# Optimization experiments

Measured on AMD Instinct MI355X. Metric: run time of the kernel, lower is better.

## Reference

```python
import jax, jax.numpy as jnp
import numpy as np

LMAX = 6; MMAX = 2
C = 128          # num_channels
H = 8            # num_heads
ALPHA = 32       # attn_alpha_channels
VAL = 16         # attn_value_channels (H*VAL == C)
HID = 64         # attn_hidden_channels
FFN = 128        # ffn_hidden_channels
NL = 4           # num_layers
CUTOFF = 12.0; NRBF = 600
AVG_DEG = 23.395238876342773
AVG_NODES = 77.81317
EPS = 1e-16

def _maps():
    idx, ls = [], []
    for l in range(LMAX + 1):
        mm = min(l, MMAX)
        for m in range(-mm, mm + 1):
            idx.append(l * l + l + m); ls.append(l)
    return np.array(idx), np.array(ls)
_M2F_np, _LOF_np = _maps()
M2F = jnp.asarray(_M2F_np)   # [KM] full-coefficient index of each m-restricted coeff
LOF = jnp.asarray(_LOF_np)   # [KM] degree l of each m-restricted coeff
KM = int(_M2F_np.shape[0])   # 29 for lmax=6, mmax=2
KF = (LMAX + 1) ** 2         # 49

def _rbf(d):
    # GaussianSmearing(0, cutoff, NRBF, width_scalar=2.0)
    off = jnp.linspace(0.0, CUTOFF, NRBF)
    coeff = -0.5 / (2.0 * (off[1] - off[0])) ** 2
    return jnp.exp(coeff * (d[:, None] - off) ** 2)

def _envelope(d):
    # PolynomialEnvelope, exponent p=5
    x = d / CUTOFF
    env = 1.0 - 21.0 * x ** 5 + 35.0 * x ** 6 - 15.0 * x ** 7
    return jnp.where(x < 1.0, env, 0.0)

def _rms(x, g):
    # merge-norm over channel dim with learned per-channel scale
    return x * jax.lax.rsqrt(jnp.mean(x * x, axis=-1, keepdims=True) + 1e-6) * g

def _forward(atomic_numbers, edge_index, edge_distance, emb,
             We0, be0, We1, be1, Weproj, gamma1, gamma2,
             Wr0, Wr1, Wrl, Wmsg, Wap, wa, Wg, Wv, Wo,
             Wf1, Wfg, Wf2, Wh1, Wh2):
    N = atomic_numbers.shape[0]
    src, tgt = edge_index[0], edge_index[1]
    rbf = _rbf(edge_distance)            # [E, NRBF]
    env = _envelope(edge_distance)       # [E]
    # node init: atom embedding on the l=0 component
    x = jnp.zeros((N, KF, C), rbf.dtype).at[:, 0, :].set(emb[atomic_numbers])
    # edge-degree embedding: radial MLP -> per-edge coeffs -> scatter to targets
    h = jax.nn.silu(rbf @ We0 + be0)
    h = jax.nn.silu(h @ We1 + be1)
    deg = (h @ Weproj).reshape(-1, KM, C)              # [E, KM, C]
    x = x.at[tgt[:, None], M2F[None, :], :].add(deg / AVG_DEG)
    for i in range(NL):
        # ---- equivariant graph attention ----
        y = _rms(x, gamma1[i])
        ym = y[:, M2F, :]                               # [N, KM, C] m-restricted
        m = jnp.concatenate([ym[src], ym[tgt]], axis=-1)  # [E, KM, 2C]
        m = jnp.einsum('ekc,ch->ekh', m, Wmsg[i])       # [E, KM, HID]
        # radial function, shared across m within each l (use_rad_l_parametrization)
        rad = jax.nn.silu(jax.nn.silu(rbf @ Wr0[i]) @ Wr1[i])
        radl = rad @ Wrl[i]                             # [E, LMAX+1]
        m = m * radl[:, LOF][..., None]
        # attention logits from invariant (l=0) part
        a = jax.nn.silu(m[:, 0, :] @ Wap[i]).reshape(-1, H, ALPHA)
        logits = jnp.einsum('eha,ha->eh', a, wa[i])     # [E, H]
        segmax = jnp.full((N, H), -jnp.inf, logits.dtype).at[tgt].max(logits)
        ex = env[:, None] * jnp.exp(logits - segmax[tgt])  # envelope-masked softmax
        den = jax.ops.segment_sum(ex, tgt, num_segments=N)
        attn = ex / (den[tgt] + EPS)                    # [E, H]
        # SwiGLU-gated equivariant values
        g = jax.nn.silu(m[:, 0, :] @ Wg[i])             # [E, H*VAL]
        v = jnp.einsum('ekh,hv->ekv', m, Wv[i]) * g[:, None, :]
        v = v.reshape(-1, KM, H, VAL) * attn[:, None, :, None]
        agg = jax.ops.segment_sum(v.reshape(-1, KM, H * VAL), tgt, num_segments=N)
        out = jnp.einsum('nkv,vc->nkc', agg, Wo[i])     # [N, KM, C]
        x = x.at[:, M2F, :].add(out)
        # ---- feed-forward (grid-MLP style SwiGLU) ----
        y = _rms(x, gamma2[i])
        gf = jax.nn.silu(y[:, 0, :] @ Wfg[i])           # [N, FFN]
        hf = jnp.einsum('nkc,cf->nkf', y, Wf1[i]) * gf[:, None, :]
        x = x + jnp.einsum('nkf,fc->nkc', hf, Wf2[i])
    # energy head on invariant part, sum-aggregated over nodes
    s = jax.nn.silu(x[:, 0, :] @ Wh1) @ Wh2             # [N, 1]
    return (jnp.sum(s) / AVG_NODES).reshape(1)

def setup_inputs() -> dict:
    key = jax.random.key(0)
    ks = jax.random.split(key, 24)
    N, E = 6000, 120000
    def rn(k, shape, scale=0.05):
        return jax.random.normal(k, shape, dtype=jnp.float32) * scale
    inp = {}
    inp['atomic_numbers'] = jax.random.randint(ks[0], (N,), 0, 128)
    inp['edge_index'] = jax.random.randint(ks[1], (2, E), 0, N)
    inp['edge_distance'] = jax.random.uniform(ks[2], (E,), minval=0.5, maxval=CUTOFF, dtype=jnp.float32)
    inp['emb'] = rn(ks[3], (128, C), 1.0)
    inp['We0'] = rn(ks[4], (NRBF, 128)); inp['be0'] = jnp.zeros((128,), jnp.float32)
    inp['We1'] = rn(ks[5], (128, 128)); inp['be1'] = jnp.zeros((128,), jnp.float32)
    inp['Weproj'] = rn(ks[6], (128, KM * C))
    inp['gamma1'] = jnp.ones((NL, C), jnp.float32)
    inp['gamma2'] = jnp.ones((NL, C), jnp.float32)
    inp['Wr0'] = rn(ks[7], (NL, NRBF, 128))
    inp['Wr1'] = rn(ks[8], (NL, 128, 128))
    inp['Wrl'] = rn(ks[9], (NL, 128, LMAX + 1), 0.1)
    inp['Wmsg'] = rn(ks[10], (NL, 2 * C, HID))
    inp['Wap'] = rn(ks[11], (NL, HID, H * ALPHA))
    inp['wa'] = rn(ks[12], (NL, H, ALPHA))
    inp['Wg'] = rn(ks[13], (NL, HID, H * VAL))
    inp['Wv'] = rn(ks[14], (NL, HID, H * VAL))
    inp['Wo'] = rn(ks[15], (NL, H * VAL, C))
    inp['Wf1'] = rn(ks[16], (NL, C, FFN))
    inp['Wfg'] = rn(ks[17], (NL, C, FFN))
    inp['Wf2'] = rn(ks[18], (NL, FFN, C))
    inp['Wh1'] = rn(ks[19], (C, C))
    inp['Wh2'] = rn(ks[20], (C, 1))
    return inp

def reference(atomic_numbers, edge_index, edge_distance, emb,
              We0, be0, We1, be1, Weproj, gamma1, gamma2,
              Wr0, Wr1, Wrl, Wmsg, Wap, wa, Wg, Wv, Wo,
              Wf1, Wfg, Wf2, Wh1, Wh2):
    return _forward(atomic_numbers, edge_index, edge_distance, emb,
                    We0, be0, We1, be1, Weproj, gamma1, gamma2,
                    Wr0, Wr1, Wrl, Wmsg, Wap, wa, Wg, Wv, Wo,
                    Wf1, Wfg, Wf2, Wh1, Wh2)
```

## Files before the change

### kernel.cpp

```cpp
#include <hip/hip_runtime.h>

#define KM 29
#define GTAB 2048

typedef __bf16 bf16_t;
typedef __bf16 bf16x8 __attribute__((ext_vector_type(8)));
typedef __bf16 bf16x4 __attribute__((ext_vector_type(4)));
typedef __bf16 bf16x2 __attribute__((ext_vector_type(2)));
typedef float  f32x4  __attribute__((ext_vector_type(4)));
typedef float  f32x2  __attribute__((ext_vector_type(2)));

__device__ __forceinline__ float silu_f(float x){ return x / (1.0f + __expf(-x)); }

__device__ __forceinline__ float wave_reduce_sum(float v){
  #pragma unroll
  for (int s = 1; s < 64; s <<= 1) v += __shfl_xor(v, s);
  return v;
}

__device__ __forceinline__ constexpr int LOF2(int k){
  return (k<1)?0 : (k<4)?1 : (k<9)?2 : (k<14)?3 : (k<19)?4 : (k<24)?5 : 6;
}

__device__ __forceinline__ f32x4 mfma16(bf16x8 a, bf16x8 b, f32x4 c){
// ... 136 lines not shown
    for (int l = 0; l < 7; l++) pl[l] = wave_reduce_sum(pl[l]);
    if (lane == 0){
      #pragma unroll
      for (int l = 0; l < 7; l++) radtab[(size_t)e*28 + i*7 + l] = pl[l];
    }
  }
}

__global__ void k_h2e(const float* __restrict__ ed, const float* __restrict__ h2tab,
                      bf16_t* __restrict__ h2e, int E){
  int idx = blockIdx.x*256 + threadIdx.x;
  if (idx >= E*128) return;
  int e = idx >> 7, ch = idx & 127;
  float d = ed[e];
  float u = d * ((GTAB-1)/12.0f);
  int j = (int)u; if (j > GTAB-2) j = GTAB-2;
  float f = u - (float)j;
  float a = h2tab[(size_t)j*128 + ch], b = h2tab[(size_t)(j+1)*128 + ch];
  h2e[idx] = (bf16_t)(a + f*(b-a));
}

__global__ __launch_bounds__(256) void k_h2sum(
    const bf16_t* __restrict__ h2e, const int* __restrict__ rowptr, const int* __restrict__ order,
    bf16_t* __restrict__ h2sum, int N)
{
  int n = blockIdx.x*2 + (threadIdx.x >> 7);
  int ch = threadIdx.x & 127;
  if (n >= N) return;
  int rp = rowptr[n], deg = rowptr[n+1] - rp;
  float acc = 0.f;
  for (int idx = 0; idx < deg; idx++){
    int e = order[rp+idx];
    acc += (float)h2e[(size_t)e*128 + ch];
  }
  h2sum[(size_t)n*128 + ch] = (bf16_t)acc;
}

__global__ __launch_bounds__(256) void k_init_x(
    const int* __restrict__ Z, const float* __restrict__ emb,
    const bf16_t* __restrict__ WeprojT, const bf16_t* __restrict__ h2sum,
    bf16_t* __restrict__ Xb, int N)
{
  __shared__ bf16_t h2s[32*136];
  __shared__ int Zs[32];
  int n0 = blockIdx.x*32, t = threadIdx.x;
  for (int idx = t; idx < 32*128; idx += 256){
    int nn = idx >> 7, ch = idx & 127;
    int n = n0 + nn;
    h2s[nn*136 + ch] = (n < N) ? h2sum[(size_t)n*128 + ch] : (bf16_t)0.f;
  }
  if (t < 32) Zs[t] = (n0 + t < N) ? Z[n0+t] : 0;
  __syncthreads();
  int wid = t >> 6, lane = t & 63;
  int mtile = wid & 1;
  int row = mtile*16 + (lane & 15);
  int koff = (lane >> 4)*8;
  bf16x8 afr[4];
  #pragma unroll
  for (int kk = 0; kk < 4; kk++) afr[kk] = *(const bf16x8*)(h2s + row*136 + kk*32 + koff);
  for (int nt = (wid>>1); nt < 232; nt += 2){
    f32x4 acc = {0.f,0.f,0.f,0.f};
    int col = nt*16 + (lane & 15);
    #pragma unroll
    for (int kk = 0; kk < 4; kk++){
      bf16x8 b = *(const bf16x8*)(WeprojT + (size_t)col*128 + kk*32 + koff);
      acc = mfma16(afr[kk], b, acc);
    }
    #pragma unroll
    for (int r = 0; r < 4; r++){
      int r32 = mtile*16 + (lane>>4)*4 + r;
      int n = n0 + r32;
      if (n < N){
        float v = acc[r] * (1.0f/23.395238876342773f);
        if (col < 128) v += emb[(size_t)Zs[r32]*128 + col];
        Xb[(size_t)n*3712 + col] = (bf16_t)v;
      }
    }
  }
}

__global__ __launch_bounds__(512) void k_pqv(
    const bf16_t* __restrict__ Xb, const float* __restrict__ gamma1,
    const bf16_t* __restrict__ WmsgCT, const bf16_t* __restrict__ WvT,
    unsigned char* __restrict__ PV8,
    float* __restrict__ P0, float* __restrict__ Q0, int layer)
{
  __shared__ bf16_t ys16[32*136];
  __shared__ bf16_t pq16[32*136];
  int n = blockIdx.x, t = threadIdx.x;
  int wid = t >> 6, lane = t & 63;
  const float* g1 = gamma1 + layer*128;
  const bf16_t* xp = Xb + (size_t)n*3712;
  for (int k = wid; k < KM; k += 8){
    float x0 = (float)xp[k*128 + lane], x1 = (float)xp[k*128 + 64 + lane];
    float ss = wave_reduce_sum(x0*x0 + x1*x1);
    float sc = rsqrtf(ss*(1.0f/128.0f) + 1e-6f);
    ys16[k*136 + lane]      = (bf16_t)(x0*sc*g1[lane]);
    ys16[k*136 + 64 + lane] = (bf16_t)(x1*sc*g1[64+lane]);
  }
  for (int idx = t; idx < 3*136; idx += 512) ys16[29*136 + idx] = (bf16_t)0.f;
  __syncthreads();
  int mtile = wid >> 2;
  int row = mtile*16 + (lane & 15);
  int koff = (lane >> 4)*8;
  {
    const bf16_t* Bc = WmsgCT + (size_t)layer*16384;
    f32x4 acc[2] = {{0,0,0,0},{0,0,0,0}};
    #pragma unroll
    for (int kk = 0; kk < 128; kk += 32){
      bf16x8 a = *(const bf16x8*)(ys16 + row*136 + kk + koff);
      #pragma unroll
      for (int u = 0; u < 2; u++){
        int col = ((wid&3)*2+u)*16 + (lane & 15);
        bf16x8 b = *(const bf16x8*)(Bc + (size_t)col*128 + kk + koff);
        acc[u] = mfma16(a, b, acc[u]);
      }
    }
    #pragma unroll
    for (int u = 0; u < 2; u++){
      int col = ((wid&3)*2+u)*16 + (lane & 15);
      #pragma unroll
      for (int r = 0; r < 4; r++){
        int r32 = mtile*16 + (lane>>4)*4 + r;
        pq16[r32*136 + col] = (bf16_t)acc[u][r];
      }
      if (mtile == 0 && (lane>>4) == 0){
        float v = acc[u][0];
        if (col < 64) P0[(size_t)n*64 + col] = v;
        else          Q0[(size_t)n*64 + col - 64] = v;
      }
    }
  }
  __syncthreads();
  {
    const bf16_t* Bt = WvT + (size_t)layer*8192;
    f32x4 acc[2] = {{0,0,0,0},{0,0,0,0}};
    #pragma unroll
    for (int kk = 0; kk < 64; kk += 32){
      bf16x8 a = *(const bf16x8*)(pq16 + row*136 + kk + koff);
      #pragma unroll
      for (int u = 0; u < 2; u++){
        int col = ((wid&3)*2+u)*16 + (lane & 15);
        bf16x8 b = *(const bf16x8*)(Bt + (size_t)col*64 + kk + koff);
        acc[u] = mfma16(a, b, acc[u]);
      }
    }
    unsigned char* pvp = PV8 + (size_t)n*4096;
    int r0i = mtile*16 + (lane>>4)*4;
    #pragma unroll
    for (int u = 0; u < 2; u++){
      int col = ((wid&3)*2+u)*16 + (lane & 15);
      float pk[4];
      #pragma unroll
      for (int r = 0; r < 4; r++){
        int r32 = r0i + r;
        pk[r] = (r32 < KM) ? acc[u][r] : 0.f;
      }
      int dw = __builtin_amdgcn_cvt_pk_fp8_f32(pk[0], pk[1], 0, false);
      dw = __builtin_amdgcn_cvt_pk_fp8_f32(pk[2], pk[3], dw, true);
      *(unsigned int*)(pvp + col*32 + r0i) = (unsigned int)dw;
    }
  }
}

__global__ __launch_bounds__(256) void k_edge_logits(
    const int* __restrict__ EI, const float* __restrict__ ed,
    const float* __restrict__ P0, const float* __restrict__ Q0,
    const float* __restrict__ radtab, const bf16_t* __restrict__ WapT, const float* __restrict__ wa,
    const bf16_t* __restrict__ WgT, float* __restrict__ logi, bf16_t* __restrict__ gate16,
    int E, int layer)
{
  __shared__ bf16_t m0s[16*72];
  __shared__ int   srcs[16], tgts[16];
  __shared__ float r0s[16];
  int t = threadIdx.x;
  int eb = blockIdx.x*16;
  if (t < 16){
    int e = eb + t;
    if (e < E){
      srcs[t] = EI[e]; tgts[t] = EI[E+e];
      float d = ed[e];
      float u = d * ((GTAB-1)/12.0f);
      int j = (int)u; if (j > GTAB-2) j = GTAB-2;
      float f = u - (float)j;
      float a = radtab[(size_t)j*28 + layer*7], b = radtab[(size_t)(j+1)*28 + layer*7];
      r0s[t] = a + f*(b-a);
    } else { srcs[t] = 0; tgts[t] = 0; r0s[t] = 0.f; }
  }
  __syncthreads();
  #pragma unroll
  for (int u = 0; u < 4; u++){
    int idx = t + u*256;
    int i = idx >> 6, j = idx & 63;
    m0s[i*72 + j] = (bf16_t)((P0[(size_t)srcs[i]*64 + j] + Q0[(size_t)tgts[i]*64 + j]) * r0s[i]);
  }
  __syncthreads();
  int wid = t >> 6, lane = t & 63;
  int l15 = lane & 15, lg = lane >> 4;
  int koff = lg*8;
  bf16x8 a0 = *(const bf16x8*)(m0s + l15*72 + koff);
  bf16x8 a1 = *(const bf16x8*)(m0s + l15*72 + 32 + koff);
  const bf16_t* Ba = WapT + (size_t)layer*16384;
  const bf16_t* Bg = WgT  + (size_t)layer*8192;
  const float* wav = wa + layer*256;
  f32x4 accA[4], accG[2];
  #pragma unroll
  for (int u = 0; u < 4; u++){
    int col = 64*wid + u*16 + l15;
    f32x4 acc = {0,0,0,0};
    acc = mfma16(a0, *(const bf16x8*)(Ba + (size_t)col*64 + koff), acc);
    acc = mfma16(a1, *(const bf16x8*)(Ba + (size_t)col*64 + 32 + koff), acc);
    accA[u] = acc;
  }
  #pragma unroll
  for (int u = 0; u < 2; u++){
    int col = 32*wid + u*16 + l15;
    f32x4 acc = {0,0,0,0};
    acc = mfma16(a0, *(const bf16x8*)(Bg + (size_t)col*64 + koff), acc);
    acc = mfma16(a1, *(const bf16x8*)(Bg + (size_t)col*64 + 32 + koff), acc);
    accG[u] = acc;
  }
  #pragma unroll
  for (int u = 0; u < 2; u++){
    int col = 32*wid + u*16 + l15;
    #pragma unroll
    for (int r = 0; r < 4; r++){
      int e = eb + lg*4 + r;
      if (e < E) gate16[(size_t)e*128 + col] = (bf16_t)silu_f(accG[u][r]);
    }
  }
  #pragma unroll
  for (int hpair = 0; hpair < 2; hpair++){
    int c0 = 64*wid + hpair*32 + l15;
    float w0 = wav[c0], w1 = wav[c0+16];
    float s[4];
    #pragma unroll
    for (int r = 0; r < 4; r++)
      s[r] = silu_f(accA[2*hpair][r])*w0 + silu_f(accA[2*hpair+1][r])*w1;
    #pragma unroll
    for (int r = 0; r < 4; r++){
      s[r] += __shfl_xor(s[r], 1);
      s[r] += __shfl_xor(s[r], 2);
      s[r] += __shfl_xor(s[r], 4);
      s[r] += __shfl_xor(s[r], 8);
    }
    if (l15 == 0){
      #pragma unroll
      for (int r = 0; r < 4; r++){
        int e = eb + lg*4 + r;
        if (e < E) logi[(size_t)e*8 + 2*wid + hpair] = s[r];
      }
    }
  }
}

#define FMA_DW(dw, kb) { \
  f32x2 lo_ = __builtin_amdgcn_cvt_pk_f32_fp8((dw), false); \
  f32x2 hi_ = __builtin_amdgcn_cvt_pk_f32_fp8((dw), true); \
  acc[(kb)]   += lo_.x * rw[LOF2((kb))]; \
  acc[(kb)+1] += lo_.y * rw[LOF2((kb)+1)]; \
  acc[(kb)+2] += hi_.x * rw[LOF2((kb)+2)]; \
  acc[(kb)+3] += hi_.y * rw[LOF2((kb)+3)]; }

__global__ __launch_bounds__(512, 4) void k_attn_ffn(
    const int* __restrict__ EI, const int* __restrict__ rowptr, const int* __restrict__ order,
    const float* __restrict__ ed,
    const bf16_t* __restrict__ WvT, const bf16_t* __restrict__ WoT,
    const unsigned char* __restrict__ PV8, const bf16_t* __restrict__ gate16,
    const float* __restrict__ logi, const float* __restrict__ radtab,
    const float* __restrict__ gamma1, const float* __restrict__ gamma2,
    const float* __restrict__ Wfg,
    const bf16_t* __restrict__ Wf1T, const bf16_t* __restrict__ Wf2T,
    const bf16_t* __restrict__ WmsgCT,
    bf16_t* __restrict__ Xb, int layer,
    unsigned char* __restrict__ PV8o, float* __restrict__ P0o, float* __restrict__ Q0o,
    int do_tail)
{
  __shared__ float  xs[3712];
  __shared__ bf16_t ysag[32*136];
  __shared__ bf16_t hsqv[32*136];
  __shared__ char   uA[4608];
  __shared__ int    esb[64], srcs[64];
  __shared__ float  denl[32];

  bf16_t* qm16 = (bf16_t*)uA;
  float*  at8  = (float*)uA;
  float*  rl7  = (float*)(uA + 2048);
  float*  pf   = (float*)uA;

  int n = blockIdx.x, t = threadIdx.x;
  int wid = t >> 6, lane = t & 63;
  int rp = rowptr[n], deg = rowptr[n+1] - rp;

  {
    const bf16x2* Xp2 = (const bf16x2*)(Xb + (size_t)n*3712);
    for (int p = t; p < 1856; p += 512){
      bf16x2 v = Xp2[p];
      xs[2*p]   = (float)v.x;
      xs[2*p+1] = (float)v.y;
    }
  }
  {
    int m0 = (deg < 64) ? deg : 64;
    if (t < m0){ int e = order[rp + t]; esb[t] = e; srcs[t] = EI[e]; }
  }
  __syncthreads();

  if (deg > 0){
    {
      const float* g1 = gamma1 + layer*128;
      for (int k = wid; k < KM; k += 8){
        float x0 = xs[k*128 + lane], x1 = xs[k*128 + 64 + lane];
        float ss = wave_reduce_sum(x0*x0 + x1*x1);
        float sc = rsqrtf(ss*(1.0f/128.0f) + 1e-6f);
        ysag[k*136 + lane]      = (bf16_t)(x0*sc*g1[lane]);
        ysag[k*136 + 64 + lane] = (bf16_t)(x1*sc*g1[64+lane]);
      }
      for (int idx = t; idx < 3*136; idx += 512) ysag[29*136 + idx] = (bf16_t)0.f;
    }
    __syncthreads();
    {
      const bf16_t* Bc = WmsgCT + (size_t)layer*16384 + (size_t)64*128;
      int mtile = wid >> 2;
      int col = (wid & 3)*16 + (lane & 15);
      int row = mtile*16 + (lane & 15);
      int koff = (lane >> 4)*8;
      f32x4 a2 = {0,0,0,0};
      #pragma unroll
      for (int kk = 0; kk < 128; kk += 32){
        bf16x8 a = *(const bf16x8*)(ysag + row*136 + kk + koff);
        bf16x8 b = *(const bf16x8*)(Bc + (size_t)col*128 + kk + koff);
        a2 = mfma16(a, b, a2);
      }
      #pragma unroll
      for (int r = 0; r < 4; r++){
        int r32 = mtile*16 + (lane>>4)*4 + r;
        qm16[r32*72 + col] = (bf16_t)a2[r];
      }
    }
    __syncthreads();
    {
      const bf16_t* Bt = WvT + (size_t)layer*8192;
      int mtile = wid >> 2, colt = (wid & 3)*2;
      int row = mtile*16 + (lane & 15);
      int koff = (lane >> 4)*8;
      f32x4 a2[2] = {{0,0,0,0},{0,0,0,0}};
      #pragma unroll
      for (int kk = 0; kk < 64; kk += 32){
        bf16x8 a = *(const bf16x8*)(qm16 + row*72 + kk + koff);
        #pragma unroll
        for (int u = 0; u < 2; u++){
          int col = (colt+u)*16 + (lane & 15);
          bf16x8 b = *(const bf16x8*)(Bt + (size_t)col*64 + kk + koff);
          a2[u] = mfma16(a, b, a2[u]);
        }
      }
      #pragma unroll
      for (int u = 0; u < 2; u++){
        int col = (colt+u)*16 + (lane & 15);
        #pragma unroll
        for (int r = 0; r < 4; r++){
          int r32 = mtile*16 + (lane>>4)*4 + r;
          hsqv[r32*136 + col] = (bf16_t)a2[u][r];
        }
      }
    }
    __syncthreads();
    int eg = t >> 7, hv = t & 127, h = hv >> 4;
    float acc[32];
    #pragma unroll
    for (int j = 0; j < 32; j++) acc[j] = 0.f;
    float S[7];
    #pragma unroll
    for (int l = 0; l < 7; l++) S[l] = 0.f;
    float dpart = 0.f;
    for (int base = 0; base < deg; base += 64){
      int ne = min(64, deg - base);
      if (base > 0){
        __syncthreads();
        if (t < ne){ int e = order[rp + base + t]; esb[t] = e; srcs[t] = EI[e]; }
        __syncthreads();
      }
      if (t < ne*8){
        int i = t >> 3, q = t & 7;
        int e = esb[i];
        float d = ed[e];
        at8[t] = env_f(d) * __expf(logi[(size_t)e*8 + q]);
        if (q < 7){
          float u = d * ((GTAB-1)/12.0f);
          int j = (int)u; if (j > GTAB-2) j = GTAB-2;
          float f = u - (float)j;
          float a = radtab[(size_t)j*28 + layer*7 + q], b = radtab[(size_t)(j+1)*28 + layer*7 + q];
          rl7[t] = a + f*(b-a);
        }
      }
      __syncthreads();
      uint4 A0 = {0,0,0,0}, A1 = {0,0,0,0}, B0 = {0,0,0,0}, B1 = {0,0,0,0};
      float gA = 0.f, gB = 0.f;
      int i = eg;
      if (i < ne){
        const uint4* p = (const uint4*)(PV8 + (size_t)srcs[i]*4096 + hv*32);
        A0 = p[0]; A1 = p[1];
        gA = (float)gate16[(size_t)esb[i]*128 + hv];
      }
      if (i + 4 < ne){
        const uint4* p = (const uint4*)(PV8 + (size_t)srcs[i+4]*4096 + hv*32);
        B0 = p[0]; B1 = p[1];
        gB = (float)gate16[(size_t)esb[i+4]*128 + hv];
      }
      while (i < ne){
        int i2 = i + 8;
        uint4 C0 = {0,0,0,0}, C1 = {0,0,0,0}; float gC = 0.f;
        if (i2 < ne){
          const uint4* p = (const uint4*)(PV8 + (size_t)srcs[i2]*4096 + hv*32);
          C0 = p[0]; C1 = p[1];
          gC = (float)gate16[(size_t)esb[i2]*128 + hv];
        }
        float ae = at8[i*8 + h];
        dpart += ae;
        float w = gA * ae;
        float rw[7];
        #pragma unroll
        for (int l = 0; l < 7; l++){ rw[l] = rl7[i*8 + l]*w; S[l] += rw[l]; }
        FMA_DW(A0.x, 0)  FMA_DW(A0.y, 4)  FMA_DW(A0.z, 8)  FMA_DW(A0.w, 12)
        FMA_DW(A1.x, 16) FMA_DW(A1.y, 20) FMA_DW(A1.z, 24) FMA_DW(A1.w, 28)
        A0 = B0; A1 = B1; gA = gB;
        B0 = C0; B1 = C1; gB = gC;
        i += 4;
      }
    }
    #pragma unroll
    for (int j = 0; j < 32; j++)
      acc[j] += (float)hsqv[j*136 + hv] * S[LOF2(j)];
    if ((hv & 15) == 0) denl[eg*8 + h] = dpart;
    __syncthreads();
    {
      float dsum = denl[h] + denl[8 + h] + denl[16 + h] + denl[24 + h];
      float inv = 1.0f/(dsum + 1e-30f);
      #pragma unroll
      for (int j = 0; j < 32; j++) acc[j] *= inv;
    }
    if (eg == 0){
      #pragma unroll
      for (int j = 0; j < 32; j++) ysag[j*136 + hv] = (bf16_t)acc[j];
    } else if (eg == 1){
      #pragma unroll
      for (int j = 0; j < 32; j++) hsqv[j*136 + hv] = (bf16_t)acc[j];
    }
    __syncthreads();
    if (eg == 2){
      #pragma unroll
      for (int j = 0; j < 32; j++) ysag[j*136 + hv] = (bf16_t)((float)ysag[j*136 + hv] + acc[j]);
    } else if (eg == 3){
      #pragma unroll
      for (int j = 0; j < 32; j++) hsqv[j*136 + hv] = (bf16_t)((float)hsqv[j*136 + hv] + acc[j]);
    }
    __syncthreads();
    for (int idx = t; idx < 32*128; idx += 512){
      int k = idx >> 7, c = idx & 127;
      ysag[k*136 + c] = (bf16_t)((float)ysag[k*136 + c] + (float)hsqv[k*136 + c]);
    }
    __syncthreads();
    {
      const bf16_t* Bt = WoT + (size_t)layer*16384;
      int mtile = wid >> 2, colt = (wid & 3)*2;
      int row = mtile*16 + (lane & 15);
      int koff = (lane >> 4)*8;
      f32x4 a2[2] = {{0,0,0,0},{0,0,0,0}};
      #pragma unroll
      for (int kk = 0; kk < 128; kk += 32){
        bf16x8 a = *(const bf16x8*)(ysag + row*136 + kk + koff);
        #pragma unroll
        for (int u = 0; u < 2; u++){
          int col = (colt+u)*16 + (lane & 15);
          bf16x8 b = *(const bf16x8*)(Bt + (size_t)col*128 + kk + koff);
          a2[u] = mfma16(a, b, a2[u]);
        }
      }
      #pragma unroll
      for (int u = 0; u < 2; u++){
        int col = (colt+u)*16 + (lane & 15);
        #pragma unroll
        for (int r = 0; r < 4; r++){
          int r32 = mtile*16 + (lane>>4)*4 + r;
          if (r32 < KM) xs[r32*128 + col] += a2[u][r];
        }
      }
    }
  }
  __syncthreads();
  const float* g2 = gamma2 + layer*128;
  for (int k = wid; k < KM; k += 8){
    float x0 = xs[k*128 + lane], x1 = xs[k*128 + 64 + lane];
    float ss = wave_reduce_sum(x0*x0 + x1*x1);
    float sc = rsqrtf(ss*(1.0f/128.0f) + 1e-6f);
    ysag[k*136 + lane]      = (bf16_t)(x0*sc*g2[lane]);
    ysag[k*136 + 64 + lane] = (bf16_t)(x1*sc*g2[64+lane]);
  }
  for (int idx = t; idx < 3*136; idx += 512) ysag[29*136 + idx] = (bf16_t)0.f;
  __syncthreads();
  {
    int part = t >> 7, f = t & 127;
    const float* Wfgp = Wfg + (size_t)layer*16384;
    float p = 0.f;
    for (int c = part*32; c < part*32 + 32; c++) p += (float)ysag[c] * Wfgp[c*128 + f];
    pf[part*128 + f] = p;
  }
  __syncthreads();
  if (t < 128) pf[512 + t] = silu_f(pf[t] + pf[128+t] + pf[256+t] + pf[384+t]);
  __syncthreads();
  {
    const bf16_t* Bt = Wf1T + (size_t)layer*16384;
    int mtile = wid >> 2, colt = (wid & 3)*2;
    int row = mtile*16 + (lane & 15);
    int koff = (lane >> 4)*8;
    f32x4 a2[2] = {{0,0,0,0},{0,0,0,0}};
    #pragma unroll
    for (int kk = 0; kk < 128; kk += 32){
      bf16x8 a = *(const bf16x8*)(ysag + row*136 + kk + koff);
      #pragma unroll
      for (int u = 0; u < 2; u++){
        int col = (colt+u)*16 + (lane & 15);
        bf16x8 b = *(const bf16x8*)(Bt + (size_t)col*128 + kk + koff);
        a2[u] = mfma16(a, b, a2[u]);
      }
    }
    #pragma unroll
    for (int u = 0; u < 2; u++){
      int col = (colt+u)*16 + (lane & 15);
      float gfc = pf[512 + col];
      #pragma unroll
      for (int r = 0; r < 4; r++){
        int r32 = mtile*16 + (lane>>4)*4 + r;
        hsqv[r32*136 + col] = (bf16_t)(a2[u][r]*gfc);
      }
    }
  }
  __syncthreads();
  {
    const bf16_t* Bt = Wf2T + (size_t)layer*16384;
    int mtile = wid >> 2, colt = (wid & 3)*2;
    int row = mtile*16 + (lane & 15);
    int koff = (lane >> 4)*8;
    f32x4 a2[2] = {{0,0,0,0},{0,0,0,0}};
    #pragma unroll
    for (int kk = 0; kk < 128; kk += 32){
      bf16x8 a = *(const bf16x8*)(hsqv + row*136 + kk + koff);
      #pragma unroll
      for (int u = 0; u < 2; u++){
        int col = (colt+u)*16 + (lane & 15);
        bf16x8 b = *(const bf16x8*)(Bt + (size_t)col*128 + kk + koff);
        a2[u] = mfma16(a, b, a2[u]);
      }
    }
    #pragma unroll
    for (int u = 0; u < 2; u++){
      int col = (colt+u)*16 + (lane & 15);
      #pragma unroll
      for (int r = 0; r < 4; r++){
        int r32 = mtile*16 + (lane>>4)*4 + r;
        if (r32 < KM) xs[r32*128 + col] += a2[u][r];
      }
    }
  }
  __syncthreads();
  {
    bf16x2* Xp2 = (bf16x2*)(Xb + (size_t)n*3712);
    for (int p = t; p < 1856; p += 512){
      bf16x2 v;
      v.x = (bf16_t)xs[2*p];
      v.y = (bf16_t)xs[2*p+1];
      Xp2[p] = v;
    }
  }
  if (do_tail){
    const float* g1n = gamma1 + (size_t)(layer+1)*128;
    for (int k = wid; k < KM; k += 8){
      float x0 = xs[k*128 + lane], x1 = xs[k*128 + 64 + lane];
      float ss = wave_reduce_sum(x0*x0 + x1*x1);
      float sc = rsqrtf(ss*(1.0f/128.0f) + 1e-6f);
      ysag[k*136 + lane]      = (bf16_t)(x0*sc*g1n[lane]);
      ysag[k*136 + 64 + lane] = (bf16_t)(x1*sc*g1n[64+lane]);
    }
    __syncthreads();
    int mtile = wid >> 2;
    int row = mtile*16 + (lane & 15);
    int koff = (lane >> 4)*8;
    {
      const bf16_t* Bc = WmsgCT + (size_t)(layer+1)*16384;
      f32x4 acc[2] = {{0,0,0,0},{0,0,0,0}};
      #pragma unroll
      for (int kk = 0; kk < 128; kk += 32){
        bf16x8 a = *(const bf16x8*)(ysag + row*136 + kk + koff);
        #pragma unroll
        for (int u = 0; u < 2; u++){
          int col = ((wid&3)*2+u)*16 + (lane & 15);
          bf16x8 b = *(const bf16x8*)(Bc + (size_t)col*128 + kk + koff);
          acc[u] = mfma16(a, b, acc[u]);
        }
      }
      #pragma unroll
      for (int u = 0; u < 2; u++){
        int col = ((wid&3)*2+u)*16 + (lane & 15);
        #pragma unroll
        for (int r = 0; r < 4; r++){
          int r32 = mtile*16 + (lane>>4)*4 + r;
          hsqv[r32*136 + col] = (bf16_t)acc[u][r];
        }
        if (mtile == 0 && (lane>>4) == 0){
          float v = acc[u][0];
          if (col < 64) P0o[(size_t)n*64 + col] = v;
          else          Q0o[(size_t)n*64 + col - 64] = v;
        }
      }
    }
    __syncthreads();
    {
      const bf16_t* Bt = WvT + (size_t)(layer+1)*8192;
      f32x4 acc[2] = {{0,0,0,0},{0,0,0,0}};
      #pragma unroll
      for (int kk = 0; kk < 64; kk += 32){
        bf16x8 a = *(const bf16x8*)(hsqv + row*136 + kk + koff);
        #pragma unroll
        for (int u = 0; u < 2; u++){
          int col = ((wid&3)*2+u)*16 + (lane & 15);
          bf16x8 b = *(const bf16x8*)(Bt + (size_t)col*64 + kk + koff);
          acc[u] = mfma16(a, b, acc[u]);
        }
      }
      unsigned char* pvp = PV8o + (size_t)n*4096;
      int r0i = mtile*16 + (lane>>4)*4;
      #pragma unroll
      for (int u = 0; u < 2; u++){
        int col = ((wid&3)*2+u)*16 + (lane & 15);
        float pk[4];
        #pragma unroll
        for (int r = 0; r < 4; r++){
          int r32 = r0i + r;
          pk[r] = (r32 < KM) ? acc[u][r] : 0.f;
        }
        int dw = __builtin_amdgcn_cvt_pk_fp8_f32(pk[0], pk[1], 0, false);
        dw = __builtin_amdgcn_cvt_pk_fp8_f32(pk[2], pk[3], dw, true);
        *(unsigned int*)(pvp + col*32 + r0i) = (unsigned int)dw;
      }
    }
  }
}

__global__ __launch_bounds__(256) void k_head(
    const bf16_t* __restrict__ Xb, const float* __restrict__ Wh1, const float* __restrict__ Wh2,
    float* __restrict__ partial, int N)
{
  __shared__ float wsum[4];
  int t = threadIdx.x;
  int half = t >> 7;
  int n = blockIdx.x*2 + half;
  int f = t & 127;
  float sv = 0.f;
  if (n < N){
    const bf16_t* xp = Xb + (size_t)n*3712;
    float acc = 0.f;
    for (int c = 0; c < 128; c++) acc += (float)xp[c]*Wh1[c*128 + f];
    sv = silu_f(acc)*Wh2[f];
  }
  sv = wave_reduce_sum(sv);
  if ((t & 63) == 0) wsum[t >> 6] = sv;
  __syncthreads();
  if (t == 0) partial[blockIdx.x] = wsum[0] + wsum[1] + wsum[2] + wsum[3];
}

__global__ __launch_bounds__(256) void k_reduce(const float* __restrict__ partial, float* __restrict__ out, int P){
  __shared__ float sh[256];
  int t = threadIdx.x;
  float s = 0.f;
  for (int i = t; i < P; i += 256) s += partial[i];
  sh[t] = s; __syncthreads();
  for (int off = 128; off > 0; off >>= 1){
    if (t < off) sh[t] += sh[t+off];
    __syncthreads();
  }
  if (t == 0) out[0] = sh[0] / 77.81317f;
}

extern "C" void kernel_launch(void* const* d_in, const int* in_sizes, int n_in,
                              void* d_out, int out_size, void* d_ws, size_t ws_size,
                              hipStream_t stream)
{
  const int*   Z      = (const int*)d_in[0];
  const int*   EI     = (const int*)d_in[1];
  const float* ed     = (const float*)d_in[2];
  const float* emb    = (const float*)d_in[3];
  const float* We0    = (const float*)d_in[4];
  const float* be0    = (const float*)d_in[5];
  const float* We1    = (const float*)d_in[6];
  const float* be1    = (const float*)d_in[7];
  const float* Weproj = (const float*)d_in[8];
  const float* gamma1 = (const float*)d_in[9];
  const float* gamma2 = (const float*)d_in[10];
  const float* Wr0    = (const float*)d_in[11];
  const float* Wr1    = (const float*)d_in[12];
  const float* Wrl    = (const float*)d_in[13];
  const float* Wmsg   = (const float*)d_in[14];
  const float* Wap    = (const float*)d_in[15];
  const float* wa     = (const float*)d_in[16];
  const float* Wg     = (const float*)d_in[17];
  const float* Wv     = (const float*)d_in[18];
  const float* Wo     = (const float*)d_in[19];
  const float* Wf1    = (const float*)d_in[20];
  const float* Wfg    = (const float*)d_in[21];
  const float* Wf2    = (const float*)d_in[22];
  const float* Wh1    = (const float*)d_in[23];
  const float* Wh2    = (const float*)d_in[24];

  const int N = in_sizes[0];
  const int E = in_sizes[2];

  float* ws = (float*)d_ws;
  size_t o = 0;
  auto alloc = [&](size_t nf){ float* p = ws + o; o += (nf + 7) & ~(size_t)7; return p; };

  bf16_t* Xb    = (bf16_t*)alloc((size_t)N*1856);
  float* P0     = alloc((size_t)N*128);
  float* Q0     = alloc((size_t)N*128);
  float* logi   = alloc((size_t)E*8);
  float* part   = alloc((size_t)((N+1)/2) + 8);
  float* radtab = alloc((size_t)GTAB*28);
  float* h2tab  = alloc((size_t)GTAB*128);
  bf16_t* h2sum = (bf16_t*)alloc((size_t)N*64);
  unsigned char* PV8 = (unsigned char*)alloc((size_t)N*2048);
  bf16_t* gate16= (bf16_t*)alloc((size_t)E*64);
  bf16_t* arena = (bf16_t*)alloc(434176);
  int* rowptr = (int*)alloc((size_t)N+8);
  int* curs   = (int*)alloc((size_t)N);
  int* order  = (int*)alloc((size_t)E);

  bf16_t* WmsgCT  = arena;
  bf16_t* WvT     = arena + 65536;
  bf16_t* WoT     = arena + 98304;
  bf16_t* Wf1T    = arena + 163840;
  bf16_t* Wf2T    = arena + 229376;
  bf16_t* WapT    = arena + 294912;
  bf16_t* WgT     = arena + 360448;
  bf16_t* WeprojT = arena + 393216;

  bf16_t* h2e = gate16;

  hipMemsetAsync(curs, 0, sizeof(int)*N, stream);
  k_count<<<(E+255)/256, 256, 0, stream>>>(EI, curs, E);
  k_scan<<<1, 1024, 0, stream>>>(curs, rowptr, N);
  k_fill<<<(E+255)/256, 256, 0, stream>>>(EI, curs, order, E);
  k_sort<<<(N+255)/256, 256, 0, stream>>>(rowptr, order, N);

  k_tr2<<<256, 256, 0, stream>>>(Wmsg, WmsgCT);
  k_tr<<<128, 256, 0, stream>>>(Wv,   WvT,  4, 64, 128, 8192);
  k_tr<<<256, 256, 0, stream>>>(Wo,   WoT,  4, 128, 128, 16384);
  k_tr<<<256, 256, 0, stream>>>(Wf1,  Wf1T, 4, 128, 128, 16384);
  k_tr<<<256, 256, 0, stream>>>(Wf2,  Wf2T, 4, 128, 128, 16384);
  k_tr<<<256, 256, 0, stream>>>(Wap,  WapT, 4, 64, 256, 16384);
  k_tr<<<128, 256, 0, stream>>>(Wg,   WgT,  4, 64, 128, 8192);
  k_tr<<<1856, 256, 0, stream>>>(Weproj, WeprojT, 1, 128, 3712, 0);

  k_tab_embed<<<GTAB/4, 256, 0, stream>>>(We0, be0, We1, be1, Wr0, Wr1, Wrl, h2tab, radtab);
  k_h2e<<<(E*128+255)/256, 256, 0, stream>>>(ed, h2tab, h2e, E);
  k_h2sum<<<(N+1)/2, 256, 0, stream>>>(h2e, rowptr, order, h2sum, N);
  k_init_x<<<(N+31)/32, 256, 0, stream>>>(Z, emb, WeprojT, h2sum, Xb, N);

  k_pqv<<<N, 512, 0, stream>>>(Xb, gamma1, WmsgCT, WvT, PV8, P0, Q0, 0);

  for (int i = 0; i < 4; i++){
    int cur = i & 1, nxt = (i+1) & 1;
    unsigned char* PV8i = PV8 + (size_t)cur*N*4096;
    unsigned char* PV8o = PV8 + (size_t)nxt*N*4096;
    float* P0i = P0 + (size_t)cur*N*64, *P0o = P0 + (size_t)nxt*N*64;
    float* Q0i = Q0 + (size_t)cur*N*64, *Q0o = Q0 + (size_t)nxt*N*64;
    k_edge_logits<<<(E+15)/16, 256, 0, stream>>>(EI, ed, P0i, Q0i, radtab, WapT, wa, WgT, logi, gate16, E, i);
    k_attn_ffn<<<N, 512, 0, stream>>>(EI, rowptr, order, ed, WvT, WoT, PV8i, gate16,
                                      logi, radtab, gamma1, gamma2, Wfg, Wf1T, Wf2T, WmsgCT,
                                      Xb, i, PV8o, P0o, Q0o, (i < 3) ? 1 : 0);
  }

  int PB = (N+1)/2;
  k_head<<<PB, 256, 0, stream>>>(Xb, Wh1, Wh2, part, N);
  k_reduce<<<1, 256, 0, stream>>>(part, (float*)d_out, PB);
}
```

Measured before the change: 2.211 ms.

## Split attention kernel into gather and node-update kernels with precomputed target values

The fused per-node attention+FFN kernel is split into two kernels. k_gather does the edge aggregation and writes a bf16 aggregate buffer; k_xupdate applies Wo, the FFN and the next-layer precompute. The target-side value projection is now computed in k_pqv/xupdate and stored as FP8 (QV8) rather than recomputed inside the attention kernel. Double-buffering of PV8/P0/Q0 is dropped, which is possible because the gather now finishes before any node update begins. The aim is lower per-kernel LDS and register pressure for better occupancy, at the cost of an extra launch per layer, an agg buffer round trip and FP8 quantization of the target term.

```diff
diff --git a/kernel.cpp b/kernel.cpp
--- a/kernel.cpp
+++ b/kernel.cpp
@@ -242,7 +242,7 @@
 __global__ __launch_bounds__(512) void k_pqv(
     const bf16_t* __restrict__ Xb, const float* __restrict__ gamma1,
     const bf16_t* __restrict__ WmsgCT, const bf16_t* __restrict__ WvT,
-    unsigned char* __restrict__ PV8,
+    unsigned char* __restrict__ PV8, unsigned char* __restrict__ QV8,
     float* __restrict__ P0, float* __restrict__ Q0, int layer)
 {
   __shared__ bf16_t ys16[32*136];
@@ -319,6 +319,35 @@
       int dw = __builtin_amdgcn_cvt_pk_fp8_f32(pk[0], pk[1], 0, false);
       dw = __builtin_amdgcn_cvt_pk_fp8_f32(pk[2], pk[3], dw, true);
       *(unsigned int*)(pvp + col*32 + r0i) = (unsigned int)dw;
+    }
+  }
+  {
+    const bf16_t* Bt = WvT + (size_t)layer*8192;
+    f32x4 acc[2] = {{0,0,0,0},{0,0,0,0}};
+    #pragma unroll
+    for (int kk = 0; kk < 64; kk += 32){
+      bf16x8 a = *(const bf16x8*)(pq16 + row*136 + 64 + kk + koff);
+      #pragma unroll
+      for (int u = 0; u < 2; u++){
+        int col = ((wid&3)*2+u)*16 + (lane & 15);
+        bf16x8 b = *(const bf16x8*)(Bt + (size_t)col*64 + kk + koff);
+        acc[u] = mfma16(a, b, acc[u]);
+      }
+    }
+    unsigned char* qvp = QV8 + (size_t)n*4096;
+    int r0i = mtile*16 + (lane>>4)*4;
+    #pragma unroll
+    for (int u = 0; u < 2; u++){
+      int col = ((wid&3)*2+u)*16 + (lane & 15);
+      float pk[4];
+      #pragma unroll
+      for (int r = 0; r < 4; r++){
+        int r32 = r0i + r;
+        pk[r] = (r32 < KM) ? acc[u][r] : 0.f;
+      }
+      int dw = __builtin_amdgcn_cvt_pk_fp8_f32(pk[0], pk[1], 0, false);
+      dw = __builtin_amdgcn_cvt_pk_fp8_f32(pk[2], pk[3], dw, true);
+      *(unsigned int*)(qvp + col*32 + r0i) = (unsigned int)dw;
     }
   }
 }
@@ -422,35 +451,145 @@
   acc[(kb)+2] += hi_.x * rw[LOF2((kb)+2)]; \
   acc[(kb)+3] += hi_.y * rw[LOF2((kb)+3)]; }
 
-__global__ __launch_bounds__(512, 4) void k_attn_ffn(
+__global__ __launch_bounds__(512, 4) void k_gather(
     const int* __restrict__ EI, const int* __restrict__ rowptr, const int* __restrict__ order,
     const float* __restrict__ ed,
-    const bf16_t* __restrict__ WvT, const bf16_t* __restrict__ WoT,
-    const unsigned char* __restrict__ PV8, const bf16_t* __restrict__ gate16,
-    const float* __restrict__ logi, const float* __restrict__ radtab,
+    const unsigned char* __restrict__ PV8, const unsigned char* __restrict__ QV8,
+    const bf16_t* __restrict__ gate16, const float* __restrict__ logi,
+    const float* __restrict__ radtab,
+    bf16_t* __restrict__ agg, int layer)
+{
+  __shared__ bf16_t mA[32*136];
+  __shared__ bf16_t mB[32*136];
+  __shared__ float at8[512];
+  __shared__ float rl7[512];
+  __shared__ int   esb[64], srcs[64];
+  __shared__ float denl[32];
+
+  int n = blockIdx.x, t = threadIdx.x;
+  int rp = rowptr[n], deg = rowptr[n+1] - rp;
+  if (deg == 0){
+    for (int idx = t; idx < 3712; idx += 512) agg[(size_t)n*3712 + idx] = (bf16_t)0.f;
+    return;
+  }
+  int eg = t >> 7, hv = t & 127, h = hv >> 4;
+  float acc[32];
+  #pragma unroll
+  for (int j = 0; j < 32; j++) acc[j] = 0.f;
+  float S[7];
+  #pragma unroll
+  for (int l = 0; l < 7; l++) S[l] = 0.f;
+  float dpart = 0.f;
+  for (int base = 0; base < deg; base += 64){
+    int ne = min(64, deg - base);
+    if (base > 0) __syncthreads();
+    if (t < ne){ int e = order[rp + base + t]; esb[t] = e; srcs[t] = EI[e]; }
+    __syncthreads();
+    if (t < ne*8){
+      int i = t >> 3, q = t & 7;
+      int e = esb[i];
+      float d = ed[e];
+      at8[t] = env_f(d) * __expf(logi[(size_t)e*8 + q]);
+      if (q < 7){
+        float u = d * ((GTAB-1)/12.0f);
+        int j = (int)u; if (j > GTAB-2) j = GTAB-2;
+        float f = u - (float)j;
+        float a = radtab[(size_t)j*28 + layer*7 + q], b = radtab[(size_t)(j+1)*28 + layer*7 + q];
+        rl7[t] = a + f*(b-a);
+      }
+    }
+    __syncthreads();
+    uint4 A0 = {0,0,0,0}, A1 = {0,0,0,0}, B0 = {0,0,0,0}, B1 = {0,0,0,0};
+    float gA = 0.f, gB = 0.f;
+    int i = eg;
+    if (i < ne){
+      const uint4* p = (const uint4*)(PV8 + (size_t)srcs[i]*4096 + hv*32);
+      A0 = p[0]; A1 = p[1];
+      gA = (float)gate16[(size_t)esb[i]*128 + hv];
+    }
+    if (i + 4 < ne){
+      const uint4* p = (const uint4*)(PV8 + (size_t)srcs[i+4]*4096 + hv*32);
+      B0 = p[0]; B1 = p[1];
+      gB = (float)gate16[(size_t)esb[i+4]*128 + hv];
+    }
+    while (i < ne){
+      int i2 = i + 8;
+      uint4 C0 = {0,0,0,0}, C1 = {0,0,0,0}; float gC = 0.f;
+      if (i2 < ne){
+        const uint4* p = (const uint4*)(PV8 + (size_t)srcs[i2]*4096 + hv*32);
+        C0 = p[0]; C1 = p[1];
+        gC = (float)gate16[(size_t)esb[i2]*128 + hv];
+      }
+      float ae = at8[i*8 + h];
+      dpart += ae;
+      float w = gA * ae;
+      float rw[7];
+      #pragma unroll
+      for (int l = 0; l < 7; l++){ rw[l] = rl7[i*8 + l]*w; S[l] += rw[l]; }
+      FMA_DW(A0.x, 0)  FMA_DW(A0.y, 4)  FMA_DW(A0.z, 8)  FMA_DW(A0.w, 12)
+      FMA_DW(A1.x, 16) FMA_DW(A1.y, 20) FMA_DW(A1.z, 24) FMA_DW(A1.w, 28)
+      A0 = B0; A1 = B1; gA = gB;
+      B0 = C0; B1 = C1; gB = gC;
+      i += 4;
+    }
+  }
+  {
+    const unsigned char* qvp = QV8 + (size_t)n*4096 + hv*32;
+    uint4 q0 = *(const uint4*)qvp;
+    uint4 q1 = *(const uint4*)(qvp + 16);
+    float rw[7];
+    #pragma unroll
+    for (int l = 0; l < 7; l++) rw[l] = S[l];
+    FMA_DW(q0.x, 0)  FMA_DW(q0.y, 4)  FMA_DW(q0.z, 8)  FMA_DW(q0.w, 12)
+    FMA_DW(q1.x, 16) FMA_DW(q1.y, 20) FMA_DW(q1.z, 24) FMA_DW(q1.w, 28)
+  }
+  if ((hv & 15) == 0) denl[eg*8 + h] = dpart;
+  __syncthreads();
+  {
+    float dsum = denl[h] + denl[8 + h] + denl[16 + h] + denl[24 + h];
+    float inv = 1.0f/(dsum + 1e-30f);
+    #pragma unroll
+    for (int j = 0; j < 32; j++) acc[j] *= inv;
+  }
+  if (eg == 0){
+    #pragma unroll
+    for (int j = 0; j < 32; j++) mA[j*136 + hv] = (bf16_t)acc[j];
+  } else if (eg == 1){
+    #pragma unroll
+    for (int j = 0; j < 32; j++) mB[j*136 + hv] = (bf16_t)acc[j];
+  }
+  __syncthreads();
+  if (eg == 2){
+    #pragma unroll
+    for (int j = 0; j < 32; j++) mA[j*136 + hv] = (bf16_t)((float)mA[j*136 + hv] + acc[j]);
+  } else if (eg == 3){
+    #pragma unroll
+    for (int j = 0; j < 32; j++) mB[j*136 + hv] = (bf16_t)((float)mB[j*136 + hv] + acc[j]);
+  }
+  __syncthreads();
+  for (int idx = t; idx < 3712; idx += 512){
+    int k = idx >> 7, c = idx & 127;
+    agg[(size_t)n*3712 + idx] = (bf16_t)((float)mA[k*136 + c] + (float)mB[k*136 + c]);
+  }
+}
+
+__global__ __launch_bounds__(512, 4) void k_xupdate(
+    const bf16_t* __restrict__ agg,
     const float* __restrict__ gamma1, const float* __restrict__ gamma2,
     const float* __restrict__ Wfg,
     const bf16_t* __restrict__ Wf1T, const bf16_t* __restrict__ Wf2T,
-    const bf16_t* __restrict__ WmsgCT,
+    const bf16_t* __restrict__ WoT, const bf16_t* __restrict__ WmsgCT, const bf16_t* __restrict__ WvT,
     bf16_t* __restrict__ Xb, int layer,
-    unsigned char* __restrict__ PV8o, float* __restrict__ P0o, float* __restrict__ Q0o,
-    int do_tail)
+    unsigned char* __restrict__ PV8o, unsigned char* __restrict__ QV8o,
+    float* __restrict__ P0o, float* __restrict__ Q0o, int do_tail)
 {
   __shared__ float  xs[3712];
   __shared__ bf16_t ysag[32*136];
   __shared__ bf16_t hsqv[32*136];
-  __shared__ char   uA[4608];
-  __shared__ int    esb[64], srcs[64];
-  __shared__ float  denl[32];
-
-  bf16_t* qm16 = (bf16_t*)uA;
-  float*  at8  = (float*)uA;
-  float*  rl7  = (float*)(uA + 2048);
-  float*  pf   = (float*)uA;
+  __shared__ float  pf[640];
 
   int n = blockIdx.x, t = threadIdx.x;
   int wid = t >> 6, lane = t & 63;
-  int rp = rowptr[n], deg = rowptr[n+1] - rp;
 
   {
     const bf16x2* Xp2 = (const bf16x2*)(Xb + (size_t)n*3712);
@@ -460,191 +599,35 @@
       xs[2*p+1] = (float)v.y;
     }
   }
-  {
-    int m0 = (deg < 64) ? deg : 64;
-    if (t < m0){ int e = order[rp + t]; esb[t] = e; srcs[t] = EI[e]; }
-  }
-  __syncthreads();
-
-  if (deg > 0){
-    {
-      const float* g1 = gamma1 + layer*128;
-      for (int k = wid; k < KM; k += 8){
-        float x0 = xs[k*128 + lane], x1 = xs[k*128 + 64 + lane];
-        float ss = wave_reduce_sum(x0*x0 + x1*x1);
-        float sc = rsqrtf(ss*(1.0f/128.0f) + 1e-6f);
-        ysag[k*136 + lane]      = (bf16_t)(x0*sc*g1[lane]);
-        ysag[k*136 + 64 + lane] = (bf16_t)(x1*sc*g1[64+lane]);
-      }
-      for (int idx = t; idx < 3*136; idx += 512) ysag[29*136 + idx] = (bf16_t)0.f;
-    }
-    __syncthreads();
-    {
-      const bf16_t* Bc = WmsgCT + (size_t)layer*16384 + (size_t)64*128;
-      int mtile = wid >> 2;
-      int col = (wid & 3)*16 + (lane & 15);
-      int row = mtile*16 + (lane & 15);
-      int koff = (lane >> 4)*8;
-      f32x4 a2 = {0,0,0,0};
-      #pragma unroll
-      for (int kk = 0; kk < 128; kk += 32){
-        bf16x8 a = *(const bf16x8*)(ysag + row*136 + kk + koff);
-        bf16x8 b = *(const bf16x8*)(Bc + (size_t)col*128 + kk + koff);
-        a2 = mfma16(a, b, a2);
-      }
+  for (int idx = t; idx < 3712; idx += 512){
+    int k = idx >> 7, c = idx & 127;
+    ysag[k*136 + c] = agg[(size_t)n*3712 + idx];
+  }
+  for (int idx = t; idx < 3*136; idx += 512) ysag[29*136 + idx] = (bf16_t)0.f;
+  __syncthreads();
+  {
+    const bf16_t* Bt = WoT + (size_t)layer*16384;
+    int mtile = wid >> 2, colt = (wid & 3)*2;
+    int row = mtile*16 + (lane & 15);
+    int koff = (lane >> 4)*8;
+    f32x4 a2[2] = {{0,0,0,0},{0,0,0,0}};
+    #pragma unroll
+    for (int kk = 0; kk < 128; kk += 32){
+      bf16x8 a = *(const bf16x8*)(ysag + row*136 + kk + koff);
+      #pragma unroll
+      for (int u = 0; u < 2; u++){
+        int col = (colt+u)*16 + (lane & 15);
+        bf16x8 b = *(const bf16x8*)(Bt + (size_t)col*128 + kk + koff);
+        a2[u] = mfma16(a, b, a2[u]);
+      }
+    }
+    #pragma unroll
+    for (int u = 0; u < 2; u++){
+      int col = (colt+u)*16 + (lane & 15);
       #pragma unroll
       for (int r = 0; r < 4; r++){
         int r32 = mtile*16 + (lane>>4)*4 + r;
-        qm16[r32*72 + col] = (bf16_t)a2[r];
-      }
-    }
-    __syncthreads();
-    {
-      const bf16_t* Bt = WvT + (size_t)layer*8192;
-      int mtile = wid >> 2, colt = (wid & 3)*2;
-      int row = mtile*16 + (lane & 15);
-      int koff = (lane >> 4)*8;
-      f32x4 a2[2] = {{0,0,0,0},{0,0,0,0}};
-      #pragma unroll
-      for (int kk = 0; kk < 64; kk += 32){
-        bf16x8 a = *(const bf16x8*)(qm16 + row*72 + kk + koff);
-        #pragma unroll
-        for (int u = 0; u < 2; u++){
-          int col = (colt+u)*16 + (lane & 15);
-          bf16x8 b = *(const bf16x8*)(Bt + (size_t)col*64 + kk + koff);
-          a2[u] = mfma16(a, b, a2[u]);
-        }
-      }
-      #pragma unroll
-      for (int u = 0; u < 2; u++){
-        int col = (colt+u)*16 + (lane & 15);
-        #pragma unroll
-        for (int r = 0; r < 4; r++){
-          int r32 = mtile*16 + (lane>>4)*4 + r;
-          hsqv[r32*136 + col] = (bf16_t)a2[u][r];
-        }
-      }
-    }
-    __syncthreads();
-    int eg = t >> 7, hv = t & 127, h = hv >> 4;
-    float acc[32];
-    #pragma unroll
-    for (int j = 0; j < 32; j++) acc[j] = 0.f;
-    float S[7];
-    #pragma unroll
-    for (int l = 0; l < 7; l++) S[l] = 0.f;
-    float dpart = 0.f;
-    for (int base = 0; base < deg; base += 64){
-      int ne = min(64, deg - base);
-      if (base > 0){
-        __syncthreads();
-        if (t < ne){ int e = order[rp + base + t]; esb[t] = e; srcs[t] = EI[e]; }
-        __syncthreads();
-      }
-      if (t < ne*8){
-        int i = t >> 3, q = t & 7;
-        int e = esb[i];
-        float d = ed[e];
-        at8[t] = env_f(d) * __expf(logi[(size_t)e*8 + q]);
-        if (q < 7){
-          float u = d * ((GTAB-1)/12.0f);
-          int j = (int)u; if (j > GTAB-2) j = GTAB-2;
-          float f = u - (float)j;
-          float a = radtab[(size_t)j*28 + layer*7 + q], b = radtab[(size_t)(j+1)*28 + layer*7 + q];
-          rl7[t] = a + f*(b-a);
-        }
-      }
-      __syncthreads();
-      uint4 A0 = {0,0,0,0}, A1 = {0,0,0,0}, B0 = {0,0,0,0}, B1 = {0,0,0,0};
-      float gA = 0.f, gB = 0.f;
-      int i = eg;
-      if (i < ne){
-        const uint4* p = (const uint4*)(PV8 + (size_t)srcs[i]*4096 + hv*32);
-        A0 = p[0]; A1 = p[1];
-        gA = (float)gate16[(size_t)esb[i]*128 + hv];
-      }
-      if (i + 4 < ne){
-        const uint4* p = (const uint4*)(PV8 + (size_t)srcs[i+4]*4096 + hv*32);
-        B0 = p[0]; B1 = p[1];
-        gB = (float)gate16[(size_t)esb[i+4]*128 + hv];
-      }
-      while (i < ne){
-        int i2 = i + 8;
-        uint4 C0 = {0,0,0,0}, C1 = {0,0,0,0}; float gC = 0.f;
-        if (i2 < ne){
-          const uint4* p = (const uint4*)(PV8 + (size_t)srcs[i2]*4096 + hv*32);
-          C0 = p[0]; C1 = p[1];
-          gC = (float)gate16[(size_t)esb[i2]*128 + hv];
-        }
-        float ae = at8[i*8 + h];
-        dpart += ae;
-        float w = gA * ae;
-        float rw[7];
-        #pragma unroll
-        for (int l = 0; l < 7; l++){ rw[l] = rl7[i*8 + l]*w; S[l] += rw[l]; }
-        FMA_DW(A0.x, 0)  FMA_DW(A0.y, 4)  FMA_DW(A0.z, 8)  FMA_DW(A0.w, 12)
-        FMA_DW(A1.x, 16) FMA_DW(A1.y, 20) FMA_DW(A1.z, 24) FMA_DW(A1.w, 28)
-        A0 = B0; A1 = B1; gA = gB;
-        B0 = C0; B1 = C1; gB = gC;
-        i += 4;
-      }
-    }
-    #pragma unroll
-    for (int j = 0; j < 32; j++)
-      acc[j] += (float)hsqv[j*136 + hv] * S[LOF2(j)];
-    if ((hv & 15) == 0) denl[eg*8 + h] = dpart;
-    __syncthreads();
-    {
-      float dsum = denl[h] + denl[8 + h] + denl[16 + h] + denl[24 + h];
-      float inv = 1.0f/(dsum + 1e-30f);
-      #pragma unroll
-      for (int j = 0; j < 32; j++) acc[j] *= inv;
-    }
-    if (eg == 0){
-      #pragma unroll
-      for (int j = 0; j < 32; j++) ysag[j*136 + hv] = (bf16_t)acc[j];
-    } else if (eg == 1){
-      #pragma unroll
-      for (int j = 0; j < 32; j++) hsqv[j*136 + hv] = (bf16_t)acc[j];
-    }
-    __syncthreads();
-    if (eg == 2){
-      #pragma unroll
-      for (int j = 0; j < 32; j++) ysag[j*136 + hv] = (bf16_t)((float)ysag[j*136 + hv] + acc[j]);
-    } else if (eg == 3){
-      #pragma unroll
-      for (int j = 0; j < 32; j++) hsqv[j*136 + hv] = (bf16_t)((float)hsqv[j*136 + hv] + acc[j]);
-    }
-    __syncthreads();
-    for (int idx = t; idx < 32*128; idx += 512){
-      int k = idx >> 7, c = idx & 127;
-      ysag[k*136 + c] = (bf16_t)((float)ysag[k*136 + c] + (float)hsqv[k*136 + c]);
-    }
-    __syncthreads();
-    {
-      const bf16_t* Bt = WoT + (size_t)layer*16384;
-      int mtile = wid >> 2, colt = (wid & 3)*2;
-      int row = mtile*16 + (lane & 15);
-      int koff = (lane >> 4)*8;
-      f32x4 a2[2] = {{0,0,0,0},{0,0,0,0}};
-      #pragma unroll
-      for (int kk = 0; kk < 128; kk += 32){
-        bf16x8 a = *(const bf16x8*)(ysag + row*136 + kk + koff);
-        #pragma unroll
-        for (int u = 0; u < 2; u++){
-          int col = (colt+u)*16 + (lane & 15);
-          bf16x8 b = *(const bf16x8*)(Bt + (size_t)col*128 + kk + koff);
-          a2[u] = mfma16(a, b, a2[u]);
-        }
-      }
-      #pragma unroll
-      for (int u = 0; u < 2; u++){
-        int col = (colt+u)*16 + (lane & 15);
-        #pragma unroll
-        for (int r = 0; r < 4; r++){
-          int r32 = mtile*16 + (lane>>4)*4 + r;
-          if (r32 < KM) xs[r32*128 + col] += a2[u][r];
-        }
+        if (r32 < KM) xs[r32*128 + col] += a2[u][r];
       }
     }
   }
@@ -802,6 +785,35 @@
         int dw = __builtin_amdgcn_cvt_pk_fp8_f32(pk[0], pk[1], 0, false);
         dw = __builtin_amdgcn_cvt_pk_fp8_f32(pk[2], pk[3], dw, true);
         *(unsigned int*)(pvp + col*32 + r0i) = (unsigned int)dw;
+      }
+    }
+    {
+      const bf16_t* Bt = WvT + (size_t)(layer+1)*8192;
+      f32x4 acc[2] = {{0,0,0,0},{0,0,0,0}};
+      #pragma unroll
+      for (int kk = 0; kk < 64; kk += 32){
+        bf16x8 a = *(const bf16x8*)(hsqv + row*136 + 64 + kk + koff);
+        #pragma unroll
+        for (int u = 0; u < 2; u++){
+          int col = ((wid&3)*2+u)*16 + (lane & 15);
+          bf16x8 b = *(const bf16x8*)(Bt + (size_t)col*64 + kk + koff);
+          acc[u] = mfma16(a, b, acc[u]);
+        }
+      }
+      unsigned char* qvp = QV8o + (size_t)n*4096;
+      int r0i = mtile*16 + (lane>>4)*4;
+      #pragma unroll
+      for (int u = 0; u < 2; u++){
+        int col = ((wid&3)*2+u)*16 + (lane & 15);
+        float pk[4];
+        #pragma unroll
+        for (int r = 0; r < 4; r++){
+          int r32 = r0i + r;
+          pk[r] = (r32 < KM) ? acc[u][r] : 0.f;
+        }
+        int dw = __builtin_amdgcn_cvt_pk_fp8_f32(pk[0], pk[1], 0, false);
+        dw = __builtin_amdgcn_cvt_pk_fp8_f32(pk[2], pk[3], dw, true);
+        *(unsigned int*)(qvp + col*32 + r0i) = (unsigned int)dw;
       }
     }
   }
@@ -880,14 +892,16 @@
   auto alloc = [&](size_t nf){ float* p = ws + o; o += (nf + 7) & ~(size_t)7; return p; };
 
   bf16_t* Xb    = (bf16_t*)alloc((size_t)N*1856);
-  float* P0     = alloc((size_t)N*128);
-  float* Q0     = alloc((size_t)N*128);
+  float* P0     = alloc((size_t)N*64);
+  float* Q0     = alloc((size_t)N*64);
   float* logi   = alloc((size_t)E*8);
   float* part   = alloc((size_t)((N+1)/2) + 8);
   float* radtab = alloc((size_t)GTAB*28);
   float* h2tab  = alloc((size_t)GTAB*128);
   bf16_t* h2sum = (bf16_t*)alloc((size_t)N*64);
-  unsigned char* PV8 = (unsigned char*)alloc((size_t)N*2048);
+  unsigned char* PV8 = (unsigned char*)alloc((size_t)N*1024);
+  unsigned char* QV8 = (unsigned char*)alloc((size_t)N*1024);
+  bf16_t* agg   = (bf16_t*)alloc((size_t)N*1856);
   bf16_t* gate16= (bf16_t*)alloc((size_t)E*64);
   bf16_t* arena = (bf16_t*)alloc(434176);
   int* rowptr = (int*)alloc((size_t)N+8);
@@ -925,18 +939,13 @@
   k_h2sum<<<(N+1)/2, 256, 0, stream>>>(h2e, rowptr, order, h2sum, N);
   k_init_x<<<(N+31)/32, 256, 0, stream>>>(Z, emb, WeprojT, h2sum, Xb, N);
 
-  k_pqv<<<N, 512, 0, stream>>>(Xb, gamma1, WmsgCT, WvT, PV8, P0, Q0, 0);
+  k_pqv<<<N, 512, 0, stream>>>(Xb, gamma1, WmsgCT, WvT, PV8, QV8, P0, Q0, 0);
 
   for (int i = 0; i < 4; i++){
-    int cur = i & 1, nxt = (i+1) & 1;
-    unsigned char* PV8i = PV8 + (size_t)cur*N*4096;
-    unsigned char* PV8o = PV8 + (size_t)nxt*N*4096;
-    float* P0i = P0 + (size_t)cur*N*64, *P0o = P0 + (size_t)nxt*N*64;
-    float* Q0i = Q0 + (size_t)cur*N*64, *Q0o = Q0 + (size_t)nxt*N*64;
-    k_edge_logits<<<(E+15)/16, 256, 0, stream>>>(EI, ed, P0i, Q0i, radtab, WapT, wa, WgT, logi, gate16, E, i);
-    k_attn_ffn<<<N, 512, 0, stream>>>(EI, rowptr, order, ed, WvT, WoT, PV8i, gate16,
-                                      logi, radtab, gamma1, gamma2, Wfg, Wf1T, Wf2T, WmsgCT,
-                                      Xb, i, PV8o, P0o, Q0o, (i < 3) ? 1 : 0);
+    k_edge_logits<<<(E+15)/16, 256, 0, stream>>>(EI, ed, P0, Q0, radtab, WapT, wa, WgT, logi, gate16, E, i);
+    k_gather<<<N, 512, 0, stream>>>(EI, rowptr, order, ed, PV8, QV8, gate16, logi, radtab, agg, i);
+    k_xupdate<<<N, 512, 0, stream>>>(agg, gamma1, gamma2, Wfg, Wf1T, Wf2T, WoT, WmsgCT, WvT,
+                                     Xb, i, PV8, QV8, P0, Q0, (i < 3) ? 1 : 0);
   }
 
   int PB = (N+1)/2;
```

After: 2.078 ms. 6.0% less time.
